# Optimization experiments

Measured on AMD Instinct MI355X. Metric: run time of the kernel, lower is better.

Reference implementation:

```python
import jax, jax.numpy as jnp
import numpy as np

B, T, C = 2, 2048, 1024
H = 16
D = C // H  # head_dim = 64


def setup_inputs() -> dict:
    key = jax.random.key(0)
    k1, k2, k3 = jax.random.split(key, 3)
    x = jax.random.normal(k1, (B, T, C), dtype=jnp.float32)
    # torch Linear(C, 3C, bias=False): y = x @ W.T; store transposed weight [C, 3C]
    w_qkv = jax.random.normal(k2, (C, 3 * C), dtype=jnp.float32) * (1.0 / np.sqrt(C))
    w_out = jax.random.normal(k3, (C, C), dtype=jnp.float32) * (1.0 / np.sqrt(C))
    return {"x": x, "w_qkv": w_qkv, "w_out": w_out}


def reference(x, w_qkv, w_out):
    b, t, c = x.shape
    qkv = jnp.einsum('btc,cd->btd', x, w_qkv)          # [B,T,3C]
    q, k, v = jnp.split(qkv, 3, axis=-1)
    # [B,T,C] -> [B,H,T,D]
    def heads(u):
        return u.reshape(b, t, H, D).transpose(0, 2, 1, 3)
    q, k, v = heads(q), heads(k), heads(v)
    scale = 1.0 / np.sqrt(D)
    attn = jnp.einsum('bhqd,bhkd->bhqk', q, k) * scale  # [B,H,T,T]
    causal = jnp.tril(jnp.ones((t, t), dtype=bool))
    attn = jnp.where(causal, attn, -jnp.inf)
    attn = jax.nn.softmax(attn, axis=-1)                # dropout p=0.0 -> identity
    out = jnp.einsum('bhqk,bhkd->bhqd', attn, v)        # [B,H,T,D]
    out = out.transpose(0, 2, 1, 3).reshape(b, t, c)
    return jnp.einsum('btc,co->bto', out, w_out)
```

## Files before the change

### kernel.cpp

```cpp
#include <hip/hip_runtime.h>
#include <hip/hip_bf16.h>
#include <stdint.h>


#define Bv 2
#define Tv 2048
#define Cv 1024
#define Hv 16
#define Dv 64
#define Mv 4096

typedef __attribute__((ext_vector_type(8))) __bf16 bf16x8;
typedef __attribute__((ext_vector_type(4))) float f32x4;
typedef __attribute__((ext_vector_type(4))) unsigned short ushort4v;

__device__ __forceinline__ unsigned short f2bs(float f) {
  union { __bf16 h; unsigned short s; } u;
  u.h = (__bf16)f;
  return u.s;
}

__device__ __forceinline__ void gload16(const void* g, void* l) {
  __builtin_amdgcn_global_load_lds(
      (__attribute__((address_space(1))) void*)(uintptr_t)g,
      (__attribute__((address_space(3))) void*)(unsigned int)(uintptr_t)l,
      16, 0, 0);
}

__device__ __forceinline__ bf16x8 ldfrag(const unsigned short* p) {
  return *reinterpret_cast<const bf16x8*>(p);
}

__global__ void __launch_bounds__(256) cast_bf16(const float* __restrict__ in,
                                                 unsigned short* __restrict__ out) {
  int i = (blockIdx.x * 256 + threadIdx.x) * 8;
  float4 a = *reinterpret_cast<const float4*>(in + i);
  float4 b = *reinterpret_cast<const float4*>(in + i + 4);
  ushort4v o0, o1;
  o0.x = f2bs(a.x); o0.y = f2bs(a.y); o0.z = f2bs(a.z); o0.w = f2bs(a.w);
  o1.x = f2bs(b.x); o1.y = f2bs(b.y); o1.z = f2bs(b.z); o1.w = f2bs(b.w);
  *reinterpret_cast<ushort4v*>(out + i) = o0;
  *reinterpret_cast<ushort4v*>(out + i + 4) = o1;
}

__global__ void __launch_bounds__(256) transcast(const float* __restrict__ in,
                                                 unsigned short* __restrict__ out,
                                                 int R, int Cc) {
  __shared__ float tile[32][33];
  int c0 = blockIdx.x * 32;
  int r0 = blockIdx.y * 32;
  int tc = threadIdx.x & 31, tr = threadIdx.x >> 5;
#pragma unroll
  for (int i = 0; i < 4; i++)
    tile[tr + i * 8][tc] = in[(size_t)(r0 + tr + i * 8) * Cc + c0 + tc];
  __syncthreads();
#pragma unroll
  for (int i = 0; i < 4; i++)
    out[(size_t)(c0 + tr + i * 8) * R + r0 + tc] = f2bs(tile[tc][tr + i * 8]);
}

template <int EPI>
__global__ void __launch_bounds__(256) gemm128(
    const unsigned short* __restrict__ A, const unsigned short* __restrict__ Bt,
    float* __restrict__ outF, unsigned short* __restrict__ qo,
    unsigned short* __restrict__ ko, unsigned short* __restrict__ vTo, int N) {
  __shared__ unsigned short la[3][4][128][8];
  __shared__ unsigned short lb[3][4][128][8];
  const int K = 1024;
  const int NT = K / 32;
  int mb = blockIdx.y * 128, nb = blockIdx.x * 128;
  int tid = threadIdx.x;
  int l = tid & 63, w = tid >> 6;
  int wr = w >> 1, wc = w & 1;
  int lr = l & 15, lg = l >> 4;
  f32x4 acc[4][4] = {};
  int c0 = tid >> 7, r0 = tid & 127;

  auto STAGE = [&](int t, int buf) {
    int kb = t * 32;
    gload16(A + (size_t)(mb + r0) * K + kb + c0 * 8, &la[buf][c0][r0][0]);
    gload16(A + (size_t)(mb + r0) * K + kb + (c0 + 2) * 8, &la[buf][c0 + 2][r0][0]);
    gload16(Bt + (size_t)(nb + r0) * K + kb + c0 * 8, &lb[buf][c0][r0][0]);
    gload16(Bt + (size_t)(nb + r0) * K + kb + (c0 + 2) * 8, &lb[buf][c0 + 2][r0][0]);
  };
  auto COMPUTE = [&](int buf) {
    bf16x8 af[4], bfr[4];
#pragma unroll
    for (int mi = 0; mi < 4; mi++) af[mi] = ldfrag(&la[buf][lg][wr * 64 + mi * 16 + lr][0]);
#pragma unroll
    for (int ni = 0; ni < 4; ni++) bfr[ni] = ldfrag(&lb[buf][lg][wc * 64 + ni * 16 + lr][0]);
#pragma unroll
    for (int mi = 0; mi < 4; mi++)
#pragma unroll
      for (int ni = 0; ni < 4; ni++)
        acc[mi][ni] = __builtin_amdgcn_mfma_f32_16x16x32_bf16(af[mi], bfr[ni], acc[mi][ni], 0, 0, 0);
  };

  STAGE(0, 0);
  STAGE(1, 1);
  for (int i = 0; i < NT - 1; ++i) {
    asm volatile("s_waitcnt vmcnt(4)" ::: "memory");
    __builtin_amdgcn_s_barrier();
    __builtin_amdgcn_sched_barrier(0);
    if (i + 2 < NT) STAGE(i + 2, (i + 2) % 3);
    COMPUTE(i % 3);
  }
  asm volatile("s_waitcnt vmcnt(0)" ::: "memory");
  __builtin_amdgcn_s_barrier();
  __builtin_amdgcn_sched_barrier(0);
  COMPUTE((NT - 1) % 3);

#pragma unroll
  for (int mi = 0; mi < 4; mi++) {
#pragma unroll
    for (int ni = 0; ni < 4; ni++) {
      int row0 = mb + wr * 64 + mi * 16 + lg * 4;
      int col = nb + wc * 64 + ni * 16 + lr;
      if (EPI == 1) {
#pragma unroll
        for (int r = 0; r < 4; r++)
          outF[(size_t)(row0 + r) * N + col] = acc[mi][ni][r];
      } else {
        int which = col >> 10, cc = col & 1023;
        int h = cc >> 6, d = cc & 63;
        int bb = row0 >> 11, t = row0 & 2047;
        size_t bh = (size_t)bb * Hv + h;
        if (which == 0) {
#pragma unroll
          for (int r = 0; r < 4; r++)
            qo[(bh * Tv + t + r) * Dv + d] = f2bs(acc[mi][ni][r]);
        } else if (which == 1) {
#pragma unroll
          for (int r = 0; r < 4; r++)
            ko[(bh * Tv + t + r) * Dv + d] = f2bs(acc[mi][ni][r]);
        } else {
          ushort4v pk;
#pragma unroll
          for (int r = 0; r < 4; r++) pk[r] = f2bs(acc[mi][ni][r]);
          *reinterpret_cast<ushort4v*>(&vTo[(bh * Dv + d) * Tv + t]) = pk;
        }
      }
    }
  }
}

__global__ void __launch_bounds__(256) flash_attn(
    const unsigned short* __restrict__ Q, const unsigned short* __restrict__ Kk,
    const unsigned short* __restrict__ Vt, unsigned short* __restrict__ O) {
  __shared__ unsigned short lK[2][8][64][8];
  __shared__ unsigned short lV[2][8][64][8];
  __shared__ unsigned short lP[4][16][72];
  int bh = blockIdx.y;
  int b = bh >> 4, h = bh & 15;
  int tid = threadIdx.x;
  int l = tid & 63, w = tid >> 6;
  int lr = l & 15, lg = l >> 4;
  const unsigned short* Qp = Q + (size_t)bh * Tv * Dv;
  const unsigned short* Kp = Kk + (size_t)bh * Tv * Dv;
  const unsigned short* Vp = Vt + (size_t)bh * Dv * Tv;
  const float Cs = 0.125f * 1.4426950408889634f;
  const float THRraw = 8.0f / Cs;
  const __bf16 kOne = (__bf16)1.0f;
  const bf16x8 vone = {kOne, kOne, kOne, kOne, kOne, kOne, kOne, kOne};
  int sr = tid & 63, sc = tid >> 6;

  for (int ph = 0; ph < 2; ++ph) {
    int qt = ph ? (31 - (int)blockIdx.x) : (int)blockIdx.x;
    int q0 = qt * 64;
    int nt = qt + 1;
    int qrow = q0 + w * 16 + lr;
    bf16x8 qf0 = ldfrag(&Qp[(size_t)qrow * Dv + lg * 8]);
    bf16x8 qf1 = ldfrag(&Qp[(size_t)qrow * Dv + 32 + lg * 8]);
    f32x4 o[4] = {};
    f32x4 lsum = {0.f, 0.f, 0.f, 0.f};
    float mrow = -1e30f;

    auto STAGE = [&](int it, int buf) {
      int k0 = it * 64;
      gload16(Kp + (size_t)(k0 + sr) * Dv + sc * 8, &lK[buf][sc][sr][0]);
      gload16(Kp + (size_t)(k0 + sr) * Dv + (sc + 4) * 8, &lK[buf][sc + 4][sr][0]);
      gload16(Vp + (size_t)sr * Tv + k0 + sc * 8, &lV[buf][sc][sr][0]);
      gload16(Vp + (size_t)sr * Tv + k0 + (sc + 4) * 8, &lV[buf][sc + 4][sr][0]);
    };

    if (ph) __syncthreads();
    STAGE(0, 0);
    int cur = 0;
    for (int it = 0; it < nt; ++it) {
      __syncthreads();
      if (it + 1 < nt) STAGE(it + 1, cur ^ 1);
      int k0 = it * 64;
      f32x4 s[4] = {};
#pragma unroll
      for (int j = 0; j < 4; ++j) {
        bf16x8 kf0 = ldfrag(&lK[cur][lg][j * 16 + lr][0]);
        s[j] = __builtin_amdgcn_mfma_f32_16x16x32_bf16(kf0, qf0, s[j], 0, 0, 0);
        bf16x8 kf1 = ldfrag(&lK[cur][4 + lg][j * 16 + lr][0]);
        s[j] = __builtin_amdgcn_mfma_f32_16x16x32_bf16(kf1, qf1, s[j], 0, 0, 0);
      }
      int qg = q0 + w * 16 + lr;
      if (it == nt - 1) {
#pragma unroll
        for (int j = 0; j < 4; ++j)
#pragma unroll
          for (int r = 0; r < 4; ++r)
            if (k0 + j * 16 + lg * 4 + r > qg) s[j][r] = -1e30f;
      }
      float v = fmaxf(fmaxf(fmaxf(s[0][0], s[0][1]), fmaxf(s[0][2], s[0][3])),
                      fmaxf(fmaxf(s[1][0], s[1][1]), fmaxf(s[1][2], s[1][3])));
      v = fmaxf(v, fmaxf(fmaxf(fmaxf(s[2][0], s[2][1]), fmaxf(s[2][2], s[2][3])),
                         fmaxf(fmaxf(s[3][0], s[3][1]), fmaxf(s[3][2], s[3][3]))));
      v = fmaxf(v, __shfl_xor(v, 16));
      v = fmaxf(v, __shfl_xor(v, 32));
      if (__any(v > mrow + THRraw)) {
        float mn = fmaxf(mrow, v);
        float al = exp2f((mrow - mn) * Cs);
        mrow = mn;
#pragma unroll
        for (int r = 0; r < 4; ++r) {
          float alr = __shfl(al, (l & 48) | (lg * 4 + r));
          lsum[r] *= alr;
#pragma unroll
          for (int nb = 0; nb < 4; ++nb) o[nb][r] *= alr;
        }
      }
#pragma unroll
      for (int j = 0; j < 4; ++j) {
        ushort4v pk;
#pragma unroll
        for (int r = 0; r < 4; ++r) pk[r] = f2bs(exp2f((s[j][r] - mrow) * Cs));
        *reinterpret_cast<ushort4v*>(&lP[w][lr][j * 16 + lg * 4]) = pk;
      }
      f32x4 srow = {0.f, 0.f, 0.f, 0.f};
#pragma unroll
      for (int kk = 0; kk < 2; ++kk) {
        bf16x8 pf = ldfrag(&lP[w][lr][kk * 32 + lg * 8]);
        srow = __builtin_amdgcn_mfma_f32_16x16x32_bf16(pf, vone, srow, 0, 0, 0);
#pragma unroll
        for (int nb = 0; nb < 4; ++nb) {
          bf16x8 vf = ldfrag(&lV[cur][kk * 4 + lg][nb * 16 + lr][0]);
          o[nb] = __builtin_amdgcn_mfma_f32_16x16x32_bf16(pf, vf, o[nb], 0, 0, 0);
        }
      }
#pragma unroll
      for (int r = 0; r < 4; ++r) lsum[r] += srow[r];
      cur ^= 1;
    }
#pragma unroll
    for (int r = 0; r < 4; ++r) {
      int t = q0 + w * 16 + lg * 4 + r;
      float inv = 1.0f / lsum[r];
      size_t rowbase = ((size_t)b * Tv + t) * Cv + h * Dv;
#pragma unroll
      for (int nb = 0; nb < 4; ++nb)
        O[rowbase + nb * 16 + lr] = f2bs(o[nb][r] * inv);
    }
  }
}

extern "C" void kernel_launch(void* const* d_in, const int* in_sizes, int n_in,
                              void* d_out, int out_size, void* d_ws, size_t ws_size,
                              hipStream_t stream) {
  const float* x = (const float*)d_in[0];
  const float* w_qkv = (const float*)d_in[1];
  const float* w_out = (const float*)d_in[2];
  float* out = (float*)d_out;
  char* ws = (char*)d_ws;
  const size_t MB = 1u << 20;
  unsigned short* xb    = (unsigned short*)(ws + 0);
  unsigned short* wqkvT = (unsigned short*)(ws + 8 * MB);
  unsigned short* woutT = (unsigned short*)(ws + 14 * MB);
  unsigned short* qb    = (unsigned short*)(ws + 16 * MB);
  unsigned short* kb    = (unsigned short*)(ws + 24 * MB);
  unsigned short* vTb   = (unsigned short*)(ws + 32 * MB);
  unsigned short* ab    = (unsigned short*)(ws + 40 * MB);

  cast_bf16<<<dim3(Mv * Cv / (256 * 8)), dim3(256), 0, stream>>>(x, xb);
  transcast<<<dim3(3072 / 32, 1024 / 32), dim3(256), 0, stream>>>(w_qkv, wqkvT, 1024, 3072);
  transcast<<<dim3(1024 / 32, 1024 / 32), dim3(256), 0, stream>>>(w_out, woutT, 1024, 1024);
  gemm128<0><<<dim3(3072 / 128, Mv / 128), dim3(256), 0, stream>>>(
      xb, wqkvT, nullptr, qb, kb, vTb, 3072);
  flash_attn<<<dim3(16, Bv * Hv), dim3(256), 0, stream>>>(qb, kb, vTb, ab);
  gemm128<1><<<dim3(Cv / 128, Mv / 128), dim3(256), 0, stream>>>(
      ab, woutT, out, nullptr, nullptr, nullptr, Cv);
}
```

Measured before the change: 141.4 us.

## Use dedicated 256x256 tile kernel for QKV projection GEMM

Replaces the templated 128x128 GEMM for the QKV projection with a 512-thread kernel computing 256x256 tiles, with a 64-wide K step and double-buffered LDS staging. The output GEMM keeps the 128x128 kernel, now without the template branch. Larger tiles raise data reuse per block and reduce global loads. The trade-off is a 192-block grid that does not fill all CUs, plus heavy LDS use that limits occupancy.

```diff
diff --git a/kernel.cpp b/kernel.cpp
--- a/kernel.cpp
+++ b/kernel.cpp
@@ -59,11 +59,83 @@
     out[(size_t)(c0 + tr + i * 8) * R + r0 + tc] = f2bs(tile[tc][tr + i * 8]);
 }
 
-template <int EPI>
+__global__ void __launch_bounds__(512, 2) gemm256_qkv(
+    const unsigned short* __restrict__ A, const unsigned short* __restrict__ Bt,
+    unsigned short* __restrict__ qo, unsigned short* __restrict__ ko,
+    unsigned short* __restrict__ vTo) {
+  __shared__ unsigned short la[2][8][256][8];
+  __shared__ unsigned short lb[2][8][256][8];
+  const int K = 1024, N = 3072;
+  int mb = blockIdx.y * 256, nb = blockIdx.x * 256;
+  int tid = threadIdx.x;
+  int l = tid & 63, w = tid >> 6;
+  int wr = w >> 2, wc = w & 3;
+  int lr = l & 15, lg = l >> 4;
+  f32x4 acc[8][4] = {};
+
+  auto STAGE = [&](int kb, int buf) {
+#pragma unroll
+    for (int p = 0; p < 4; ++p) {
+      int slot = tid + 512 * p;
+      int c = slot >> 8, r = slot & 255;
+      gload16(A + (size_t)(mb + r) * K + kb + c * 8, &la[buf][c][r][0]);
+      gload16(Bt + (size_t)(nb + r) * K + kb + c * 8, &lb[buf][c][r][0]);
+    }
+  };
+
+  STAGE(0, 0);
+  int cur = 0;
+  for (int kb = 0; kb < K; kb += 64) {
+    __syncthreads();
+    if (kb + 64 < K) STAGE(kb + 64, cur ^ 1);
+#pragma unroll
+    for (int ks = 0; ks < 2; ++ks) {
+      bf16x8 bfr[4];
+#pragma unroll
+      for (int ni = 0; ni < 4; ni++)
+        bfr[ni] = ldfrag(&lb[cur][ks * 4 + lg][wc * 64 + ni * 16 + lr][0]);
+#pragma unroll
+      for (int mi = 0; mi < 8; mi++) {
+        bf16x8 af = ldfrag(&la[cur][ks * 4 + lg][wr * 128 + mi * 16 + lr][0]);
+#pragma unroll
+        for (int ni = 0; ni < 4; ni++)
+          acc[mi][ni] = __builtin_amdgcn_mfma_f32_16x16x32_bf16(af, bfr[ni], acc[mi][ni], 0, 0, 0);
+      }
+    }
+    cur ^= 1;
+  }
+
+#pragma unroll
+  for (int mi = 0; mi < 8; mi++) {
+#pragma unroll
+    for (int ni = 0; ni < 4; ni++) {
+      int row0 = mb + wr * 128 + mi * 16 + lg * 4;
+      int col = nb + wc * 64 + ni * 16 + lr;
+      int which = col >> 10, cc = col & 1023;
+      int h = cc >> 6, d = cc & 63;
+      int bb = row0 >> 11, t = row0 & 2047;
+      size_t bh = (size_t)bb * Hv + h;
+      if (which == 0) {
+#pragma unroll
+        for (int r = 0; r < 4; r++)
+          qo[(bh * Tv + t + r) * Dv + d] = f2bs(acc[mi][ni][r]);
+      } else if (which == 1) {
+#pragma unroll
+        for (int r = 0; r < 4; r++)
+          ko[(bh * Tv + t + r) * Dv + d] = f2bs(acc[mi][ni][r]);
+      } else {
+        ushort4v pk;
+#pragma unroll
+        for (int r = 0; r < 4; r++) pk[r] = f2bs(acc[mi][ni][r]);
+        *reinterpret_cast<ushort4v*>(&vTo[(bh * Dv + d) * Tv + t]) = pk;
+      }
+    }
+  }
+}
+
 __global__ void __launch_bounds__(256) gemm128(
     const unsigned short* __restrict__ A, const unsigned short* __restrict__ Bt,
-    float* __restrict__ outF, unsigned short* __restrict__ qo,
-    unsigned short* __restrict__ ko, unsigned short* __restrict__ vTo, int N) {
+    float* __restrict__ outF, int N) {
   __shared__ unsigned short la[3][4][128][8];
   __shared__ unsigned short lb[3][4][128][8];
   const int K = 1024;
@@ -116,30 +188,9 @@
     for (int ni = 0; ni < 4; ni++) {
       int row0 = mb + wr * 64 + mi * 16 + lg * 4;
       int col = nb + wc * 64 + ni * 16 + lr;
-      if (EPI == 1) {
-#pragma unroll
-        for (int r = 0; r < 4; r++)
-          outF[(size_t)(row0 + r) * N + col] = acc[mi][ni][r];
-      } else {
-        int which = col >> 10, cc = col & 1023;
-        int h = cc >> 6, d = cc & 63;
-        int bb = row0 >> 11, t = row0 & 2047;
-        size_t bh = (size_t)bb * Hv + h;
-        if (which == 0) {
-#pragma unroll
-          for (int r = 0; r < 4; r++)
-            qo[(bh * Tv + t + r) * Dv + d] = f2bs(acc[mi][ni][r]);
-        } else if (which == 1) {
-#pragma unroll
-          for (int r = 0; r < 4; r++)
-            ko[(bh * Tv + t + r) * Dv + d] = f2bs(acc[mi][ni][r]);
-        } else {
-          ushort4v pk;
-#pragma unroll
-          for (int r = 0; r < 4; r++) pk[r] = f2bs(acc[mi][ni][r]);
-          *reinterpret_cast<ushort4v*>(&vTo[(bh * Dv + d) * Tv + t]) = pk;
-        }
-      }
+#pragma unroll
+      for (int r = 0; r < 4; r++)
+        outF[(size_t)(row0 + r) * N + col] = acc[mi][ni][r];
     }
   }
 }
@@ -278,9 +329,8 @@
   cast_bf16<<<dim3(Mv * Cv / (256 * 8)), dim3(256), 0, stream>>>(x, xb);
   transcast<<<dim3(3072 / 32, 1024 / 32), dim3(256), 0, stream>>>(w_qkv, wqkvT, 1024, 3072);
   transcast<<<dim3(1024 / 32, 1024 / 32), dim3(256), 0, stream>>>(w_out, woutT, 1024, 1024);
-  gemm128<0><<<dim3(3072 / 128, Mv / 128), dim3(256), 0, stream>>>(
-      xb, wqkvT, nullptr, qb, kb, vTb, 3072);
+  gemm256_qkv<<<dim3(3072 / 256, Mv / 256), dim3(512), 0, stream>>>(
+      xb, wqkvT, qb, kb, vTb);
   flash_attn<<<dim3(16, Bv * Hv), dim3(256), 0, stream>>>(qb, kb, vTb, ab);
-  gemm128<1><<<dim3(Cv / 128, Mv / 128), dim3(256), 0, stream>>>(
-      ab, woutT, out, nullptr, nullptr, nullptr, Cv);
-}
+  gemm128<<<dim3(Cv / 128, Mv / 128), dim3(256), 0, stream>>>(ab, woutT, out, Cv);
+}
```

Result: slower. 152.6 us (+7.9%).

## Load K/V fragments directly from global memory, one query tile per block

Applied to the files above, without the earlier changes.

Drops the LDS double-buffered K/V staging and its barriers, so each wave reads its K and V MFMA fragments straight from global memory (relying on L1/L2 for reuse across the four waves). It also replaces the paired causal-balancing tiles per block with one tile per block over a doubled grid, longest tiles first. This removes block-level synchronisation and LDS traffic, but each wave now issues redundant global loads, which raises cache pressure and exposes load latency with no explicit prefetch.

```diff
diff --git a/kernel.cpp b/kernel.cpp
--- a/kernel.cpp
+++ b/kernel.cpp
@@ -147,8 +147,6 @@
 __global__ void __launch_bounds__(256) flash_attn(
     const unsigned short* __restrict__ Q, const unsigned short* __restrict__ Kk,
     const unsigned short* __restrict__ Vt, unsigned short* __restrict__ O) {
-  __shared__ unsigned short lK[2][8][64][8];
-  __shared__ unsigned short lV[2][8][64][8];
   __shared__ unsigned short lP[4][16][72];
   int bh = blockIdx.y;
   int b = bh >> 4, h = bh & 15;
@@ -162,99 +160,86 @@
   const float THRraw = 8.0f / Cs;
   const __bf16 kOne = (__bf16)1.0f;
   const bf16x8 vone = {kOne, kOne, kOne, kOne, kOne, kOne, kOne, kOne};
-  int sr = tid & 63, sc = tid >> 6;
-
-  for (int ph = 0; ph < 2; ++ph) {
-    int qt = ph ? (31 - (int)blockIdx.x) : (int)blockIdx.x;
-    int q0 = qt * 64;
-    int nt = qt + 1;
-    int qrow = q0 + w * 16 + lr;
-    bf16x8 qf0 = ldfrag(&Qp[(size_t)qrow * Dv + lg * 8]);
-    bf16x8 qf1 = ldfrag(&Qp[(size_t)qrow * Dv + 32 + lg * 8]);
-    f32x4 o[4] = {};
-    f32x4 lsum = {0.f, 0.f, 0.f, 0.f};
-    float mrow = -1e30f;
-
-    auto STAGE = [&](int it, int buf) {
-      int k0 = it * 64;
-      gload16(Kp + (size_t)(k0 + sr) * Dv + sc * 8, &lK[buf][sc][sr][0]);
-      gload16(Kp + (size_t)(k0 + sr) * Dv + (sc + 4) * 8, &lK[buf][sc + 4][sr][0]);
-      gload16(Vp + (size_t)sr * Tv + k0 + sc * 8, &lV[buf][sc][sr][0]);
-      gload16(Vp + (size_t)sr * Tv + k0 + (sc + 4) * 8, &lV[buf][sc + 4][sr][0]);
-    };
-
-    if (ph) __syncthreads();
-    STAGE(0, 0);
-    int cur = 0;
-    for (int it = 0; it < nt; ++it) {
-      __syncthreads();
-      if (it + 1 < nt) STAGE(it + 1, cur ^ 1);
-      int k0 = it * 64;
-      f32x4 s[4] = {};
-#pragma unroll
-      for (int j = 0; j < 4; ++j) {
-        bf16x8 kf0 = ldfrag(&lK[cur][lg][j * 16 + lr][0]);
-        s[j] = __builtin_amdgcn_mfma_f32_16x16x32_bf16(kf0, qf0, s[j], 0, 0, 0);
-        bf16x8 kf1 = ldfrag(&lK[cur][4 + lg][j * 16 + lr][0]);
-        s[j] = __builtin_amdgcn_mfma_f32_16x16x32_bf16(kf1, qf1, s[j], 0, 0, 0);
+
+  int qt = 31 - (int)blockIdx.x;
+  int q0 = qt * 64;
+  int nt = qt + 1;
+  int qrow = q0 + w * 16 + lr;
+  bf16x8 qf0 = ldfrag(&Qp[(size_t)qrow * Dv + lg * 8]);
+  bf16x8 qf1 = ldfrag(&Qp[(size_t)qrow * Dv + 32 + lg * 8]);
+  f32x4 o[4] = {};
+  f32x4 lsum = {0.f, 0.f, 0.f, 0.f};
+  float mrow = -1e30f;
+
+  for (int it = 0; it < nt; ++it) {
+    int k0 = it * 64;
+    f32x4 s[4] = {};
+#pragma unroll
+    for (int j = 0; j < 4; ++j) {
+      bf16x8 kf0 = ldfrag(&Kp[(size_t)(k0 + j * 16 + lr) * Dv + lg * 8]);
+      s[j] = __builtin_amdgcn_mfma_f32_16x16x32_bf16(kf0, qf0, s[j], 0, 0, 0);
+      bf16x8 kf1 = ldfrag(&Kp[(size_t)(k0 + j * 16 + lr) * Dv + 32 + lg * 8]);
+      s[j] = __builtin_amdgcn_mfma_f32_16x16x32_bf16(kf1, qf1, s[j], 0, 0, 0);
+    }
+    bf16x8 vf[2][4];
+#pragma unroll
+    for (int kk = 0; kk < 2; ++kk)
+#pragma unroll
+      for (int nb = 0; nb < 4; ++nb)
+        vf[kk][nb] = ldfrag(&Vp[(size_t)(nb * 16 + lr) * Tv + k0 + kk * 32 + lg * 8]);
+    int qg = q0 + w * 16 + lr;
+    if (it == nt - 1) {
+#pragma unroll
+      for (int j = 0; j < 4; ++j)
+#pragma unroll
+        for (int r = 0; r < 4; ++r)
+          if (k0 + j * 16 + lg * 4 + r > qg) s[j][r] = -1e30f;
+    }
+    float v = fmaxf(fmaxf(fmaxf(s[0][0], s[0][1]), fmaxf(s[0][2], s[0][3])),
+                    fmaxf(fmaxf(s[1][0], s[1][1]), fmaxf(s[1][2], s[1][3])));
+    v = fmaxf(v, fmaxf(fmaxf(fmaxf(s[2][0], s[2][1]), fmaxf(s[2][2], s[2][3])),
+                       fmaxf(fmaxf(s[3][0], s[3][1]), fmaxf(s[3][2], s[3][3]))));
+    v = fmaxf(v, __shfl_xor(v, 16));
+    v = fmaxf(v, __shfl_xor(v, 32));
+    if (__any(v > mrow + THRraw)) {
+      float mn = fmaxf(mrow, v);
+      float al = exp2f((mrow - mn) * Cs);
+      mrow = mn;
+#pragma unroll
+      for (int r = 0; r < 4; ++r) {
+        float alr = __shfl(al, (l & 48) | (lg * 4 + r));
+        lsum[r] *= alr;
+#pragma unroll
+        for (int nb = 0; nb < 4; ++nb) o[nb][r] *= alr;
       }
-      int qg = q0 + w * 16 + lr;
-      if (it == nt - 1) {
-#pragma unroll
-        for (int j = 0; j < 4; ++j)
-#pragma unroll
-          for (int r = 0; r < 4; ++r)
-            if (k0 + j * 16 + lg * 4 + r > qg) s[j][r] = -1e30f;
-      }
-      float v = fmaxf(fmaxf(fmaxf(s[0][0], s[0][1]), fmaxf(s[0][2], s[0][3])),
-                      fmaxf(fmaxf(s[1][0], s[1][1]), fmaxf(s[1][2], s[1][3])));
-      v = fmaxf(v, fmaxf(fmaxf(fmaxf(s[2][0], s[2][1]), fmaxf(s[2][2], s[2][3])),
-                         fmaxf(fmaxf(s[3][0], s[3][1]), fmaxf(s[3][2], s[3][3]))));
-      v = fmaxf(v, __shfl_xor(v, 16));
-      v = fmaxf(v, __shfl_xor(v, 32));
-      if (__any(v > mrow + THRraw)) {
-        float mn = fmaxf(mrow, v);
-        float al = exp2f((mrow - mn) * Cs);
-        mrow = mn;
-#pragma unroll
-        for (int r = 0; r < 4; ++r) {
-          float alr = __shfl(al, (l & 48) | (lg * 4 + r));
-          lsum[r] *= alr;
-#pragma unroll
-          for (int nb = 0; nb < 4; ++nb) o[nb][r] *= alr;
-        }
-      }
-#pragma unroll
-      for (int j = 0; j < 4; ++j) {
-        ushort4v pk;
-#pragma unroll
-        for (int r = 0; r < 4; ++r) pk[r] = f2bs(exp2f((s[j][r] - mrow) * Cs));
-        *reinterpret_cast<ushort4v*>(&lP[w][lr][j * 16 + lg * 4]) = pk;
-      }
-      f32x4 srow = {0.f, 0.f, 0.f, 0.f};
-#pragma unroll
-      for (int kk = 0; kk < 2; ++kk) {
-        bf16x8 pf = ldfrag(&lP[w][lr][kk * 32 + lg * 8]);
-        srow = __builtin_amdgcn_mfma_f32_16x16x32_bf16(pf, vone, srow, 0, 0, 0);
-#pragma unroll
-        for (int nb = 0; nb < 4; ++nb) {
-          bf16x8 vf = ldfrag(&lV[cur][kk * 4 + lg][nb * 16 + lr][0]);
-          o[nb] = __builtin_amdgcn_mfma_f32_16x16x32_bf16(pf, vf, o[nb], 0, 0, 0);
-        }
-      }
-#pragma unroll
-      for (int r = 0; r < 4; ++r) lsum[r] += srow[r];
-      cur ^= 1;
-    }
-#pragma unroll
-    for (int r = 0; r < 4; ++r) {
-      int t = q0 + w * 16 + lg * 4 + r;
-      float inv = 1.0f / lsum[r];
-      size_t rowbase = ((size_t)b * Tv + t) * Cv + h * Dv;
+    }
+#pragma unroll
+    for (int j = 0; j < 4; ++j) {
+      ushort4v pk;
+#pragma unroll
+      for (int r = 0; r < 4; ++r) pk[r] = f2bs(exp2f((s[j][r] - mrow) * Cs));
+      *reinterpret_cast<ushort4v*>(&lP[w][lr][j * 16 + lg * 4]) = pk;
+    }
+    f32x4 srow = {0.f, 0.f, 0.f, 0.f};
+#pragma unroll
+    for (int kk = 0; kk < 2; ++kk) {
+      bf16x8 pf = ldfrag(&lP[w][lr][kk * 32 + lg * 8]);
+      srow = __builtin_amdgcn_mfma_f32_16x16x32_bf16(pf, vone, srow, 0, 0, 0);
 #pragma unroll
       for (int nb = 0; nb < 4; ++nb)
-        O[rowbase + nb * 16 + lr] = f2bs(o[nb][r] * inv);
-    }
+        o[nb] = __builtin_amdgcn_mfma_f32_16x16x32_bf16(pf, vf[kk][nb], o[nb], 0, 0, 0);
+    }
+#pragma unroll
+    for (int r = 0; r < 4; ++r) lsum[r] += srow[r];
+  }
+#pragma unroll
+  for (int r = 0; r < 4; ++r) {
+    int t = q0 + w * 16 + lg * 4 + r;
+    float inv = 1.0f / lsum[r];
+    size_t rowbase = ((size_t)b * Tv + t) * Cv + h * Dv;
+#pragma unroll
+    for (int nb = 0; nb < 4; ++nb)
+      O[rowbase + nb * 16 + lr] = f2bs(o[nb][r] * inv);
   }
 }
 
@@ -280,7 +265,7 @@
   transcast<<<dim3(1024 / 32, 1024 / 32), dim3(256), 0, stream>>>(w_out, woutT, 1024, 1024);
   gemm128<0><<<dim3(3072 / 128, Mv / 128), dim3(256), 0, stream>>>(
       xb, wqkvT, nullptr, qb, kb, vTb, 3072);
-  flash_attn<<<dim3(16, Bv * Hv), dim3(256), 0, stream>>>(qb, kb, vTb, ab);
+  flash_attn<<<dim3(32, Bv * Hv), dim3(256), 0, stream>>>(qb, kb, vTb, ab);
   gemm128<1><<<dim3(Cv / 128, Mv / 128), dim3(256), 0, stream>>>(
       ab, woutT, out, nullptr, nullptr, nullptr, Cv);
 }
```

After: 318.4 us. 2.25x slower.
